# Kernel tuning notes

Measured on AMD Instinct MI355X. Metric: run time of the kernel, lower is better.

## Reference

```python
import jax, jax.numpy as jnp
import numpy as np

# cls_loss defaults from DetectionLoss.cls_loss
ALPHA = 0.75
GAMMA = 2.0
NUM_NEG = 10000   # negatives randomly subsampled per sample
NUM_HARD = 100    # hard negatives kept when there are no positives
RATIO = 100       # neg:pos hard-mining ratio

B = 8
N = 64 * 128 * 128  # anchor points for crop_size=[64,128,128]


def setup_inputs() -> dict:
    key = jax.random.key(0)
    k1, k2, k3, k4 = jax.random.split(key, 4)
    # logits, biased negative so sigmoid ~ small background prob
    pred = jax.random.normal(k1, (B, N, 1), jnp.float32) * 2.0 - 4.0
    # sparse binary targets: ~50 positive voxels per sample
    target = (jax.random.uniform(k2, (B, N, 1)) < 5e-5).astype(jnp.float32)
    # ignore mask: 0 = use, -1 = ignore (as written by target_proprocess)
    mask_ignore = -(jax.random.uniform(k3, (B, N, 1)) < 1e-3).astype(jnp.float32)
    # deterministic replacement for random.sample over negative indices:
    # per-sample random permutation prefix (without replacement)
    perm = jax.vmap(lambda k: jax.random.permutation(k, N)[:NUM_NEG])(
        jax.random.split(k4, B))
    return {"pred": pred, "target": target, "mask_ignore": mask_ignore,
            "neg_idx": perm.astype(jnp.int32)}


def _per_sample_loss(pred_b, target_b, mask_b, idx):
    # pred_b/target_b/mask_b: (N,1); idx: (NUM_NEG,)
    pred_b = pred_b[:, 0]
    target_b = target_b[:, 0]
    mask_b = mask_b[:, 0]
    # focal weight uses detached probabilities (pred_b.detach() in torch)
    prob = jnp.clip(jax.nn.sigmoid(jax.lax.stop_gradient(pred_b)), 1e-4, 1.0 - 1e-4)
    pos = target_b == 1.0
    alpha_f = jnp.where(pos, ALPHA, 1.0 - ALPHA)
    focal_w = alpha_f * jnp.where(pos, 1.0 - prob, prob) ** GAMMA
    # numerically stable BCE-with-logits, reduction='none'
    bce = jnp.maximum(pred_b, 0.0) - pred_b * target_b + jnp.log1p(jnp.exp(-jnp.abs(pred_b)))
    loss = jnp.where(mask_b == 0.0, focal_w * bce, 0.0)
    # false-negative boost (only positives can match, so safe unconditionally)
    loss = jnp.where(pos & (prob < 0.8), 4.0 * loss, loss)

    num_pos = jnp.sum(pos)
    pos_sum = jnp.sum(jnp.where(pos, loss, 0.0))

    # gather the NUM_NEG randomly subsampled candidates; mask out any index
    # that accidentally hits a positive with sentinel -1 (losses are >= 0)
    neg_vals = jnp.where(pos[idx], -1.0, loss[idx])          # (NUM_NEG,)
    sorted_desc = jnp.sort(neg_vals)[::-1]                    # descending
    # k = min(ratio*num_pos, NUM_NEG) if positives exist else NUM_HARD
    k = jnp.where(num_pos > 0, jnp.minimum(RATIO * num_pos, NUM_NEG), NUM_HARD)
    keep = (jnp.arange(NUM_NEG) < k) & (sorted_desc >= 0.0)
    neg_sum = jnp.sum(jnp.where(keep, sorted_desc, 0.0))

    return (pos_sum + neg_sum) / jnp.maximum(num_pos.astype(jnp.float32), 1.0)


def reference(pred, target, mask_ignore, neg_idx):
    losses = jax.vmap(_per_sample_loss)(pred, target, mask_ignore, neg_idx)
    return jnp.mean(losses)
```

## Files before the change

kernel.cpp:

```cpp
#include <hip/hip_runtime.h>
#include <math.h>

namespace {

constexpr float kAlpha   = 0.75f;
constexpr int   kNumNeg  = 10000;
constexpr int   kNumHard = 100;
constexpr int   kRatio   = 100;
constexpr int   kB       = 8;
constexpr int   kN       = 64 * 128 * 128;
constexpr int   kTpb1    = 256;
constexpr int   kGatherBlocks = (kB * kNumNeg + kTpb1 - 1) / kTpb1;
constexpr int   kSlices  = 256;
constexpr int   kPosBlocks = kB * kSlices;
constexpr int   kTpbSel  = 1024;
constexpr int   kWavesSel = kTpbSel / 64;
constexpr int   kVPerThread = (kNumNeg + kTpbSel - 1) / kTpbSel;
constexpr unsigned kSentinel = 0xFFFFFFFFu;

__device__ __forceinline__ float loss_at(float pred, float target, float mask) {
    float prob = 1.0f / (1.0f + expf(-pred));
    prob = fminf(fmaxf(prob, 1.0e-4f), 1.0f - 1.0e-4f);
    bool pos = (target == 1.0f);
    float alpha_f = pos ? kAlpha : (1.0f - kAlpha);
    float pt = pos ? (1.0f - prob) : prob;
    float focal_w = alpha_f * pt * pt;
    float bce = fmaxf(pred, 0.0f) - pred * target + log1pf(expf(-fabsf(pred)));
    float loss = (mask == 0.0f) ? focal_w * bce : 0.0f;
    if (pos && prob < 0.8f) loss *= 4.0f;
    return loss;
}

__global__ void __launch_bounds__(kTpb1) stage1_kernel(
        const float* __restrict__ pred, const float* __restrict__ target,
        const float* __restrict__ mask, const int* __restrict__ neg_idx,
        float* __restrict__ partials, unsigned* __restrict__ gvals,
        unsigned* __restrict__ counter) {
    const int blk = blockIdx.x;
    if (blk == 0 && threadIdx.x == 0) *counter = 0u;

    if (blk < kGatherBlocks) {
        const int t = blk * kTpb1 + threadIdx.x;
        if (t < kB * kNumNeg) {
            const int b = t / kNumNeg;
            const int j = t - b * kNumNeg;
            const size_t base = (size_t)b * kN;
            const int gi = neg_idx[(size_t)b * kNumNeg + j];
            const float tg = target[base + gi];
            unsigned outv;
            if (tg == 1.0f) {
                outv = kSentinel;
            } else {
                float v = loss_at(pred[base + gi], tg, mask[base + gi]);
                outv = __float_as_uint(v);
            }
            gvals[(size_t)b * kNumNeg + j] = outv;
        }
        return;
    }

    const int pb = blk - kGatherBlocks;
    const int b = pb >> 8;
    const int slice = pb & 255;
    const size_t base = (size_t)b * kN;
    const float4* t4 = (const float4*)(target + base);
    const int tb = slice * kTpb1 + threadIdx.x;
    constexpr int kStride = kSlices * kTpb1;
    float4 v0 = t4[tb];
    float4 v1 = t4[tb + kStride];
    float4 v2 = t4[tb + 2 * kStride];
    float4 v3 = t4[tb + 3 * kStride];

    float cnt = 0.0f, psum = 0.0f;
    const float4 vv[4] = {v0, v1, v2, v3};
    #pragma unroll
    for (int it = 0; it < 4; ++it) {
        const int i = tb + it * kStride;
        float tvv[4] = {vv[it].x, vv[it].y, vv[it].z, vv[it].w};
        #pragma unroll
        for (int c = 0; c < 4; ++c) {
            if (tvv[c] == 1.0f) {
                int gi = i * 4 + c;
                cnt += 1.0f;
                psum += loss_at(pred[base + gi], 1.0f, mask[base + gi]);
            }
        }
    }
    #pragma unroll
    for (int off = 32; off > 0; off >>= 1) {
        cnt  += __shfl_down(cnt, off);
        psum += __shfl_down(psum, off);
    }
    __shared__ float sc[kTpb1 / 64], sp[kTpb1 / 64];
    const int wave = threadIdx.x / 64, lane = threadIdx.x % 64;
    if (lane == 0) { sc[wave] = cnt; sp[wave] = psum; }
    __syncthreads();
    if (threadIdx.x == 0) {
        float c = 0.0f, p = 0.0f;
        for (int w = 0; w < kTpb1 / 64; ++w) { c += sc[w]; p += sp[w]; }
        float* slot = partials + ((size_t)b * kSlices + slice) * 2;
        slot[0] = c; slot[1] = p;
    }
}

__global__ void __launch_bounds__(kTpbSel) select_kernel(
        const unsigned* __restrict__ gvals, const float* __restrict__ partials,
        float* __restrict__ batch_loss, unsigned* __restrict__ counter,
        float* __restrict__ out) {
    __shared__ unsigned whist[kWavesSel][256];
    __shared__ unsigned hist_total[256];
    __shared__ unsigned sfx[256];
    __shared__ float r0[kWavesSel], r1[kWavesSel], r2[kWavesSel], r3[kWavesSel];
    __shared__ float red[kWavesSel];
    __shared__ float sh_np, sh_ps;
    __shared__ unsigned sh_krem, sh_prefix;
    __shared__ int sh_done;

    const int b = blockIdx.x;
    const int tid = threadIdx.x;
    const int wave = tid >> 6, lane = tid & 63;

    for (int i = tid; i < kWavesSel * 256; i += kTpbSel)
        ((unsigned*)whist)[i] = 0u;
    __syncthreads();

    unsigned vreg[kVPerThread];
    float mcnt = 0.0f, msum = 0.0f;
    #pragma unroll
    for (int it = 0; it < kVPerThread; ++it) {
        const int j = tid + it * kTpbSel;
        unsigned v = kSentinel;
        if (j < kNumNeg) v = gvals[(size_t)b * kNumNeg + j];
        vreg[it] = v;
        if (v != kSentinel) {
            mcnt += 1.0f;
            msum += __uint_as_float(v);
            atomicAdd(&whist[wave][v >> 24], 1u);
        }
    }
    float c = 0.0f, p = 0.0f;
    if (tid < kSlices) {
        const float* slot = partials + ((size_t)b * kSlices + tid) * 2;
        c = slot[0]; p = slot[1];
    }
    #pragma unroll
    for (int off = 32; off > 0; off >>= 1) {
        mcnt += __shfl_down(mcnt, off);
        msum += __shfl_down(msum, off);
        c    += __shfl_down(c, off);
        p    += __shfl_down(p, off);
    }
    if (lane == 0) { r0[wave] = mcnt; r1[wave] = msum; r2[wave] = c; r3[wave] = p; }
    __syncthreads();
    float my_loss = 0.0f;
    if (tid == 0) {
        float a0 = 0, a1 = 0, a2 = 0, a3 = 0;
        for (int w = 0; w < kWavesSel; ++w) { a0 += r0[w]; a1 += r1[w]; a2 += r2[w]; a3 += r3[w]; }
        sh_np = a2; sh_ps = a3;
        const int num_pos = (int)a2;
        const int m = (int)a0;
        const int k = (num_pos > 0) ? min(kRatio * num_pos, kNumNeg) : kNumHard;
        if (k >= m) {
            my_loss = (a3 + a1) / fmaxf(a2, 1.0f);
            sh_done = 1;
        } else {
            sh_done = 0;
            sh_krem = (unsigned)k;
            sh_prefix = 0u;
        }
    }
    __syncthreads();

    if (!sh_done) {
        #pragma unroll
        for (int pass = 0; pass < 4; ++pass) {
            const int shift = 24 - 8 * pass;
            if (pass > 0) {
                for (int i = tid; i < kWavesSel * 256; i += kTpbSel)
                    ((unsigned*)whist)[i] = 0u;
                __syncthreads();
                const unsigned pmask = 0xFFFFFFFFu << (shift + 8);
                const unsigned pval = sh_prefix;
                #pragma unroll
                for (int it = 0; it < kVPerThread; ++it) {
                    unsigned v = vreg[it];
                    if (v != kSentinel && (v & pmask) == pval)
                        atomicAdd(&whist[wave][(v >> shift) & 255u], 1u);
                }
            }
            __syncthreads();
            if (tid < 256) {
                unsigned h = 0;
                #pragma unroll
                for (int w = 0; w < kWavesSel; ++w) h += whist[w][tid];
                hist_total[tid] = h;
            }
            __syncthreads();
            if (wave == 0) {
                unsigned v0 = hist_total[255 - (4 * lane + 0)];
                unsigned v1 = hist_total[255 - (4 * lane + 1)];
                unsigned v2 = hist_total[255 - (4 * lane + 2)];
                unsigned v3 = hist_total[255 - (4 * lane + 3)];
                unsigned p0 = v0, p1 = p0 + v1, p2 = p1 + v2, p3 = p2 + v3;
                unsigned acc = p3;
                #pragma unroll
                for (int off = 1; off < 64; off <<= 1) {
                    unsigned y = __shfl_up(acc, off);
                    if (lane >= off) acc += y;
                }
                unsigned excl = acc - p3;
                sfx[255 - (4 * lane + 0)] = excl + p0;
                sfx[255 - (4 * lane + 1)] = excl + p1;
                sfx[255 - (4 * lane + 2)] = excl + p2;
                sfx[255 - (4 * lane + 3)] = excl + p3;
            }
            __syncthreads();
            const unsigned krem = sh_krem;
            __syncthreads();
            if (tid < 256) {
                unsigned si = sfx[tid];
                bool sel = (si >= krem) && (tid == 255 || sfx[tid + 1] < krem);
                if (sel) {
                    sh_krem = krem - (si - hist_total[tid]);
                    sh_prefix |= (unsigned)tid << shift;
                }
            }
            __syncthreads();
        }

        const unsigned tbits = sh_prefix;
        float gsum = 0.0f;
        #pragma unroll
        for (int it = 0; it < kVPerThread; ++it) {
            unsigned v = vreg[it];
            if (v != kSentinel && v > tbits) gsum += __uint_as_float(v);
        }
        #pragma unroll
        for (int off = 32; off > 0; off >>= 1) gsum += __shfl_down(gsum, off);
        if (lane == 0) red[wave] = gsum;
        __syncthreads();
        if (tid == 0) {
            float sum_gt = 0.0f;
            for (int w = 0; w < kWavesSel; ++w) sum_gt += red[w];
            const float tval = __uint_as_float(sh_prefix);
            const float neg_sum = sum_gt + (float)sh_krem * tval;
            my_loss = (sh_ps + neg_sum) / fmaxf(sh_np, 1.0f);
        }
    }

    if (tid == 0) {
        __hip_atomic_store(&batch_loss[b], my_loss, __ATOMIC_RELEASE,
                           __HIP_MEMORY_SCOPE_AGENT);
        unsigned old = __hip_atomic_fetch_add(counter, 1u, __ATOMIC_ACQ_REL,
                                              __HIP_MEMORY_SCOPE_AGENT);
        if (old == (unsigned)(kB - 1)) {
            float s = 0.0f;
            for (int i = 0; i < kB; ++i)
                s += __hip_atomic_load(&batch_loss[i], __ATOMIC_ACQUIRE,
                                       __HIP_MEMORY_SCOPE_AGENT);
            out[0] = s / (float)kB;
        }
    }
}

}

extern "C" void kernel_launch(void* const* d_in, const int* in_sizes, int n_in,
                              void* d_out, int out_size, void* d_ws, size_t ws_size,
                              hipStream_t stream) {
    const float* pred   = (const float*)d_in[0];
    const float* target = (const float*)d_in[1];
    const float* mask   = (const float*)d_in[2];
    const int*   negidx = (const int*)d_in[3];
    float* ws = (float*)d_ws;
    float*    partials   = ws;
    float*    batch_loss = ws + 4096;
    unsigned* counter    = (unsigned*)(ws + 4104);
    unsigned* gvals      = (unsigned*)(ws + 4112);
    float* out = (float*)d_out;

    stage1_kernel<<<dim3(kGatherBlocks + kPosBlocks), dim3(kTpb1), 0, stream>>>(
        pred, target, mask, negidx, partials, gvals, counter);
    select_kernel<<<dim3(kB), dim3(kTpbSel), 0, stream>>>(
        gvals, partials, batch_loss, counter, out);
}
```

Measured before the change: 28.99 us.

## Fuse gather, positive scan and selection into one kernel with last-block-done handoff

Merges the two kernels into a single launch. Each batch's gather and streaming blocks bump a per-batch atomic counter, and the last block to finish runs the radix-select and final reduction for that batch. Blocks grow to 1024 threads with 64 stream slices per batch. This removes a kernel launch boundary and lets batches whose inputs are ready start selection early, but adds a hipMemsetAsync to reset the counters and loses occupancy by using large blocks for the streaming scan.

```diff
diff --git a/kernel.cpp b/kernel.cpp
--- a/kernel.cpp
+++ b/kernel.cpp
@@ -9,14 +9,21 @@
 constexpr int   kRatio   = 100;
 constexpr int   kB       = 8;
 constexpr int   kN       = 64 * 128 * 128;
-constexpr int   kTpb1    = 256;
-constexpr int   kGatherBlocks = (kB * kNumNeg + kTpb1 - 1) / kTpb1;
-constexpr int   kSlices  = 256;
-constexpr int   kPosBlocks = kB * kSlices;
-constexpr int   kTpbSel  = 1024;
-constexpr int   kWavesSel = kTpbSel / 64;
-constexpr int   kVPerThread = (kNumNeg + kTpbSel - 1) / kTpbSel;
+constexpr int   kTpb     = 1024;
+constexpr int   kWaves   = kTpb / 64;
+constexpr int   kGatherPerB = 10;
+constexpr int   kStreamPerB = 64;
+constexpr int   kPerB    = kGatherPerB + kStreamPerB;
+constexpr int   kGatherBlocks = kB * kGatherPerB;
+constexpr int   kGrid    = kGatherBlocks + kB * kStreamPerB;
+constexpr int   kVPer    = (kNumNeg + kTpb - 1) / kTpb;
 constexpr unsigned kSentinel = 0xFFFFFFFFu;
+
+constexpr int oPartials  = 0;
+constexpr int oBatchLoss = 1024;
+constexpr int oCnt       = 1032;
+constexpr int oGCnt      = 1040;
+constexpr int oGvals     = 1536;
 
 __device__ __forceinline__ float loss_at(float pred, float target, float mask) {
     float prob = 1.0f / (1.0f + expf(-pred));
@@ -31,19 +38,28 @@
     return loss;
 }
 
-__global__ void __launch_bounds__(kTpb1) stage1_kernel(
+__global__ void __launch_bounds__(kTpb) fused_kernel(
         const float* __restrict__ pred, const float* __restrict__ target,
         const float* __restrict__ mask, const int* __restrict__ neg_idx,
-        float* __restrict__ partials, unsigned* __restrict__ gvals,
-        unsigned* __restrict__ counter) {
+        unsigned* __restrict__ ws, float* __restrict__ out) {
     const int blk = blockIdx.x;
-    if (blk == 0 && threadIdx.x == 0) *counter = 0u;
-
+    const int tid = threadIdx.x;
+    const int wave = tid >> 6, lane = tid & 63;
+    float* wsf = (float*)ws;
+
+    __shared__ unsigned whist[kWaves][256];
+    __shared__ unsigned hist_total[256], sfx[256];
+    __shared__ float sA[kWaves], sB[kWaves];
+    __shared__ float sh_np, sh_ps;
+    __shared__ unsigned sh_krem, sh_prefix;
+    __shared__ int sh_done, sh_last;
+
+    int b;
     if (blk < kGatherBlocks) {
-        const int t = blk * kTpb1 + threadIdx.x;
-        if (t < kB * kNumNeg) {
-            const int b = t / kNumNeg;
-            const int j = t - b * kNumNeg;
+        b = blk / kGatherPerB;
+        const int sub = blk % kGatherPerB;
+        const int j = sub * kTpb + tid;
+        if (j < kNumNeg) {
             const size_t base = (size_t)b * kN;
             const int gi = neg_idx[(size_t)b * kNumNeg + j];
             const float tg = target[base + gi];
@@ -54,83 +70,73 @@
                 float v = loss_at(pred[base + gi], tg, mask[base + gi]);
                 outv = __float_as_uint(v);
             }
-            gvals[(size_t)b * kNumNeg + j] = outv;
-        }
-        return;
-    }
-
-    const int pb = blk - kGatherBlocks;
-    const int b = pb >> 8;
-    const int slice = pb & 255;
-    const size_t base = (size_t)b * kN;
-    const float4* t4 = (const float4*)(target + base);
-    const int tb = slice * kTpb1 + threadIdx.x;
-    constexpr int kStride = kSlices * kTpb1;
-    float4 v0 = t4[tb];
-    float4 v1 = t4[tb + kStride];
-    float4 v2 = t4[tb + 2 * kStride];
-    float4 v3 = t4[tb + 3 * kStride];
-
-    float cnt = 0.0f, psum = 0.0f;
-    const float4 vv[4] = {v0, v1, v2, v3};
-    #pragma unroll
-    for (int it = 0; it < 4; ++it) {
-        const int i = tb + it * kStride;
-        float tvv[4] = {vv[it].x, vv[it].y, vv[it].z, vv[it].w};
-        #pragma unroll
-        for (int c = 0; c < 4; ++c) {
-            if (tvv[c] == 1.0f) {
-                int gi = i * 4 + c;
-                cnt += 1.0f;
-                psum += loss_at(pred[base + gi], 1.0f, mask[base + gi]);
-            }
-        }
-    }
-    #pragma unroll
-    for (int off = 32; off > 0; off >>= 1) {
-        cnt  += __shfl_down(cnt, off);
-        psum += __shfl_down(psum, off);
-    }
-    __shared__ float sc[kTpb1 / 64], sp[kTpb1 / 64];
-    const int wave = threadIdx.x / 64, lane = threadIdx.x % 64;
-    if (lane == 0) { sc[wave] = cnt; sp[wave] = psum; }
-    __syncthreads();
-    if (threadIdx.x == 0) {
-        float c = 0.0f, p = 0.0f;
-        for (int w = 0; w < kTpb1 / 64; ++w) { c += sc[w]; p += sp[w]; }
-        float* slot = partials + ((size_t)b * kSlices + slice) * 2;
-        slot[0] = c; slot[1] = p;
-    }
-}
-
-__global__ void __launch_bounds__(kTpbSel) select_kernel(
-        const unsigned* __restrict__ gvals, const float* __restrict__ partials,
-        float* __restrict__ batch_loss, unsigned* __restrict__ counter,
-        float* __restrict__ out) {
-    __shared__ unsigned whist[kWavesSel][256];
-    __shared__ unsigned hist_total[256];
-    __shared__ unsigned sfx[256];
-    __shared__ float r0[kWavesSel], r1[kWavesSel], r2[kWavesSel], r3[kWavesSel];
-    __shared__ float red[kWavesSel];
-    __shared__ float sh_np, sh_ps;
-    __shared__ unsigned sh_krem, sh_prefix;
-    __shared__ int sh_done;
-
-    const int b = blockIdx.x;
-    const int tid = threadIdx.x;
-    const int wave = tid >> 6, lane = tid & 63;
-
-    for (int i = tid; i < kWavesSel * 256; i += kTpbSel)
+            ws[oGvals + b * kNumNeg + j] = outv;
+        }
+    } else {
+        const int s = blk - kGatherBlocks;
+        b = s >> 6;
+        const int slice = s & 63;
+        const size_t base = (size_t)b * kN;
+        const float4* t4 = (const float4*)(target + base);
+        const int tb = slice * kTpb + tid;
+        constexpr int kStride = kStreamPerB * kTpb;
+        float4 v0 = t4[tb];
+        float4 v1 = t4[tb + kStride];
+        float4 v2 = t4[tb + 2 * kStride];
+        float4 v3 = t4[tb + 3 * kStride];
+
+        float cnt = 0.0f, psum = 0.0f;
+        const float4 vv[4] = {v0, v1, v2, v3};
+        #pragma unroll
+        for (int it = 0; it < 4; ++it) {
+            const int i = tb + it * kStride;
+            float tvv[4] = {vv[it].x, vv[it].y, vv[it].z, vv[it].w};
+            #pragma unroll
+            for (int c = 0; c < 4; ++c) {
+                if (tvv[c] == 1.0f) {
+                    int gi = i * 4 + c;
+                    cnt += 1.0f;
+                    psum += loss_at(pred[base + gi], 1.0f, mask[base + gi]);
+                }
+            }
+        }
+        #pragma unroll
+        for (int off = 32; off > 0; off >>= 1) {
+            cnt  += __shfl_down(cnt, off);
+            psum += __shfl_down(psum, off);
+        }
+        if (lane == 0) { sA[wave] = cnt; sB[wave] = psum; }
+        __syncthreads();
+        if (tid == 0) {
+            float c = 0.0f, p = 0.0f;
+            for (int w = 0; w < kWaves; ++w) { c += sA[w]; p += sB[w]; }
+            float* slot = wsf + oPartials + ((size_t)b * kStreamPerB + slice) * 2;
+            slot[0] = c; slot[1] = p;
+        }
+    }
+
+    __syncthreads();
+    if (tid == 0) {
+        __threadfence();
+        unsigned old = __hip_atomic_fetch_add(&ws[oCnt + b], 1u,
+                                              __ATOMIC_ACQ_REL,
+                                              __HIP_MEMORY_SCOPE_AGENT);
+        sh_last = (old == (unsigned)(kPerB - 1));
+    }
+    __syncthreads();
+    if (!sh_last) return;
+
+    for (int i = tid; i < kWaves * 256; i += kTpb)
         ((unsigned*)whist)[i] = 0u;
     __syncthreads();
 
-    unsigned vreg[kVPerThread];
+    unsigned vreg[kVPer];
     float mcnt = 0.0f, msum = 0.0f;
     #pragma unroll
-    for (int it = 0; it < kVPerThread; ++it) {
-        const int j = tid + it * kTpbSel;
+    for (int it = 0; it < kVPer; ++it) {
+        const int j = tid + it * kTpb;
         unsigned v = kSentinel;
-        if (j < kNumNeg) v = gvals[(size_t)b * kNumNeg + j];
+        if (j < kNumNeg) v = ws[oGvals + b * kNumNeg + j];
         vreg[it] = v;
         if (v != kSentinel) {
             mcnt += 1.0f;
@@ -139,8 +145,8 @@
         }
     }
     float c = 0.0f, p = 0.0f;
-    if (tid < kSlices) {
-        const float* slot = partials + ((size_t)b * kSlices + tid) * 2;
+    if (tid < kStreamPerB) {
+        const float* slot = wsf + oPartials + ((size_t)b * kStreamPerB + tid) * 2;
         c = slot[0]; p = slot[1];
     }
     #pragma unroll
@@ -150,12 +156,13 @@
         c    += __shfl_down(c, off);
         p    += __shfl_down(p, off);
     }
+    __shared__ float r0[kWaves], r1[kWaves], r2[kWaves], r3[kWaves];
     if (lane == 0) { r0[wave] = mcnt; r1[wave] = msum; r2[wave] = c; r3[wave] = p; }
     __syncthreads();
     float my_loss = 0.0f;
     if (tid == 0) {
         float a0 = 0, a1 = 0, a2 = 0, a3 = 0;
-        for (int w = 0; w < kWavesSel; ++w) { a0 += r0[w]; a1 += r1[w]; a2 += r2[w]; a3 += r3[w]; }
+        for (int w = 0; w < kWaves; ++w) { a0 += r0[w]; a1 += r1[w]; a2 += r2[w]; a3 += r3[w]; }
         sh_np = a2; sh_ps = a3;
         const int num_pos = (int)a2;
         const int m = (int)a0;
@@ -176,13 +183,13 @@
         for (int pass = 0; pass < 4; ++pass) {
             const int shift = 24 - 8 * pass;
             if (pass > 0) {
-                for (int i = tid; i < kWavesSel * 256; i += kTpbSel)
+                for (int i = tid; i < kWaves * 256; i += kTpb)
                     ((unsigned*)whist)[i] = 0u;
                 __syncthreads();
                 const unsigned pmask = 0xFFFFFFFFu << (shift + 8);
                 const unsigned pval = sh_prefix;
                 #pragma unroll
-                for (int it = 0; it < kVPerThread; ++it) {
+                for (int it = 0; it < kVPer; ++it) {
                     unsigned v = vreg[it];
                     if (v != kSentinel && (v & pmask) == pval)
                         atomicAdd(&whist[wave][(v >> shift) & 255u], 1u);
@@ -192,7 +199,7 @@
             if (tid < 256) {
                 unsigned h = 0;
                 #pragma unroll
-                for (int w = 0; w < kWavesSel; ++w) h += whist[w][tid];
+                for (int w = 0; w < kWaves; ++w) h += whist[w][tid];
                 hist_total[tid] = h;
             }
             __syncthreads();
@@ -231,17 +238,17 @@
         const unsigned tbits = sh_prefix;
         float gsum = 0.0f;
         #pragma unroll
-        for (int it = 0; it < kVPerThread; ++it) {
+        for (int it = 0; it < kVPer; ++it) {
             unsigned v = vreg[it];
             if (v != kSentinel && v > tbits) gsum += __uint_as_float(v);
         }
         #pragma unroll
         for (int off = 32; off > 0; off >>= 1) gsum += __shfl_down(gsum, off);
-        if (lane == 0) red[wave] = gsum;
+        if (lane == 0) r0[wave] = gsum;
         __syncthreads();
         if (tid == 0) {
             float sum_gt = 0.0f;
-            for (int w = 0; w < kWavesSel; ++w) sum_gt += red[w];
+            for (int w = 0; w < kWaves; ++w) sum_gt += r0[w];
             const float tval = __uint_as_float(sh_prefix);
             const float neg_sum = sum_gt + (float)sh_krem * tval;
             my_loss = (sh_ps + neg_sum) / fmaxf(sh_np, 1.0f);
@@ -249,15 +256,15 @@
     }
 
     if (tid == 0) {
-        __hip_atomic_store(&batch_loss[b], my_loss, __ATOMIC_RELEASE,
-                           __HIP_MEMORY_SCOPE_AGENT);
-        unsigned old = __hip_atomic_fetch_add(counter, 1u, __ATOMIC_ACQ_REL,
+        __hip_atomic_store((float*)&wsf[oBatchLoss + b], my_loss,
+                           __ATOMIC_RELEASE, __HIP_MEMORY_SCOPE_AGENT);
+        unsigned old = __hip_atomic_fetch_add(&ws[oGCnt], 1u, __ATOMIC_ACQ_REL,
                                               __HIP_MEMORY_SCOPE_AGENT);
         if (old == (unsigned)(kB - 1)) {
             float s = 0.0f;
             for (int i = 0; i < kB; ++i)
-                s += __hip_atomic_load(&batch_loss[i], __ATOMIC_ACQUIRE,
-                                       __HIP_MEMORY_SCOPE_AGENT);
+                s += __hip_atomic_load((float*)&wsf[oBatchLoss + i],
+                                       __ATOMIC_ACQUIRE, __HIP_MEMORY_SCOPE_AGENT);
             out[0] = s / (float)kB;
         }
     }
@@ -272,15 +279,10 @@
     const float* target = (const float*)d_in[1];
     const float* mask   = (const float*)d_in[2];
     const int*   negidx = (const int*)d_in[3];
-    float* ws = (float*)d_ws;
-    float*    partials   = ws;
-    float*    batch_loss = ws + 4096;
-    unsigned* counter    = (unsigned*)(ws + 4104);
-    unsigned* gvals      = (unsigned*)(ws + 4112);
+    unsigned* ws = (unsigned*)d_ws;
     float* out = (float*)d_out;
 
-    stage1_kernel<<<dim3(kGatherBlocks + kPosBlocks), dim3(kTpb1), 0, stream>>>(
-        pred, target, mask, negidx, partials, gvals, counter);
-    select_kernel<<<dim3(kB), dim3(kTpbSel), 0, stream>>>(
-        gvals, partials, batch_loss, counter, out);
-}
+    hipMemsetAsync((char*)d_ws + oCnt * 4, 0, (oGCnt - oCnt + 1) * 4, stream);
+    fused_kernel<<<dim3(kGrid), dim3(kTpb), 0, stream>>>(pred, target, mask,
+                                                         negidx, ws, out);
+}
```

After: 71.47 us. +146.5%, slower.
